# Kernel optimization log

Measured on AMD Instinct MI355X. Metric: run time of the kernel, lower is better.

The kernel has to match this reference:

```python
import jax, jax.numpy as jnp
import numpy as np

N_ENT = 100000
N_REL = 237
DIM = 128
N_EDGE = 500000
BATCH = 4096


def setup_inputs() -> dict:
    key = jax.random.key(0)
    ks = jax.random.split(key, 13)
    s = 0.05
    return {
        "edge_index": jax.random.randint(ks[0], (2, N_EDGE), 0, N_ENT, dtype=jnp.int32),
        "edge_type": jax.random.randint(ks[1], (N_EDGE,), 0, 2 * N_REL, dtype=jnp.int32),
        "sub": jax.random.randint(ks[2], (BATCH,), 0, N_ENT, dtype=jnp.int32),
        "rel": jax.random.randint(ks[3], (BATCH,), 0, 2 * N_REL, dtype=jnp.int32),
        "init_embed_real": jax.random.normal(ks[4], (N_ENT, DIM), jnp.float32) * s,
        "init_embed_imag": jax.random.normal(ks[5], (N_ENT, DIM), jnp.float32) * s,
        "init_rel_real": jax.random.normal(ks[6], (2 * N_REL, DIM), jnp.float32) * s,
        "init_rel_imag": jax.random.normal(ks[7], (2 * N_REL, DIM), jnp.float32) * s,
        "im_proj": jax.random.normal(ks[8], (DIM, DIM), jnp.float32) * s,
        "w_real": jax.random.normal(ks[9], (DIM, DIM), jnp.float32) * s,
        "w_imag": jax.random.normal(ks[10], (DIM, DIM), jnp.float32) * s,
        "w_rel": jax.random.normal(ks[11], (DIM, DIM), jnp.float32) * s,
        "att_a": jax.random.normal(ks[12], (2 * DIM,), jnp.float32) * s,
    }


def _compram_conv(edge_index, edge_type, ent_r, ent_i, rel_r, rel_i,
                  w_real, w_imag, w_rel, att_a):
    """Relational graph-attention conv: complex (ComplEx-style) composition of
    source-entity and relation embeddings per edge, linear projection,
    edge attention with per-destination softmax (segment ops = SpecialSpmm),
    scatter-sum aggregation, tanh activation."""
    src, dst = edge_index[0], edge_index[1]
    er, ei = ent_r[src], ent_i[src]            # [E, D] gathers (irregular)
    rr, ri = rel_r[edge_type], rel_i[edge_type]
    # complex multiplication composition
    m_r = er * rr - ei * ri
    m_i = er * ri + ei * rr
    h_r = m_r @ w_real                          # [E, D]
    h_i = m_i @ w_imag
    logit = jax.nn.leaky_relu(jnp.concatenate([h_r, h_i], axis=-1) @ att_a, 0.2)
    seg_max = jax.ops.segment_max(logit, dst, num_segments=ent_r.shape[0])
    ex = jnp.exp(logit - seg_max[dst])
    denom = jax.ops.segment_sum(ex, dst, num_segments=ent_r.shape[0])
    att = ex / (denom[dst] + 1e-10)             # softmax over incoming edges
    out_r = jax.ops.segment_sum(att[:, None] * h_r, dst, num_segments=ent_r.shape[0])
    out_i = jax.ops.segment_sum(att[:, None] * h_i, dst, num_segments=ent_r.shape[0])
    out_r = jnp.tanh(out_r)
    out_i = jnp.tanh(out_i)
    rel_out_r = jnp.tanh(rel_r @ w_rel)
    rel_out_i = jnp.tanh(rel_i @ w_rel)
    return out_r, out_i, rel_out_r, rel_out_i


def reference(edge_index, edge_type, sub, rel,
              init_embed_real, init_embed_imag,
              init_rel_real, init_rel_imag,
              im_proj, w_real, w_imag, w_rel, att_a):
    # imaginary parts projected through im_proj (as in forward_base)
    rel_i = init_rel_imag @ im_proj
    ent_i = init_embed_imag @ im_proj
    # single CompRAM layer (gcn_layer == 1); dropout is identity in eval mode
    e_r, e_i, r_r, r_i = _compram_conv(edge_index, edge_type,
                                       init_embed_real, ent_i,
                                       init_rel_real, rel_i,
                                       w_real, w_imag, w_rel, att_a)
    sub_r = e_r[sub]
    sub_i = e_i[sub]
    rel_r = r_r[rel]
    rel_i_q = r_i[rel]
    return sub_r, sub_i, rel_r, rel_i_q, e_r, e_i
```

## Files before the change

### kernel.cpp

```cpp
#include <hip/hip_runtime.h>
#include <hip/hip_bf16.h>

#define N_ENT   100000
#define N_RELT  474
#define DIM     128
#define N_EDGE  500000
#define BATCH_Q 4096

typedef __attribute__((ext_vector_type(8))) short short8v;
typedef __attribute__((ext_vector_type(4))) float f32x4;

#define OUT_SUBR 0
#define OUT_SUBI (BATCH_Q * DIM)
#define OUT_RELR (2 * BATCH_Q * DIM)
#define OUT_RELI (3 * BATCH_Q * DIM)
#define OUT_ER   (4 * BATCH_Q * DIM)
#define OUT_EI   (OUT_ER + N_ENT * DIM)

#define WS_ENTI  0
#define WS_RELI  (N_ENT * DIM)
#define WS_RELOR (WS_RELI + N_RELT * DIM)
#define WS_RELOI (WS_RELOR + N_RELT * DIM)
#define WS_DENOM (WS_RELOI + N_RELT * DIM)
#define WS_LIST  (WS_DENOM + N_ENT)
#define WS_CNT2  (WS_LIST + 16384)
#define WS_BSUM  (WS_CNT2 + 64)
#define WS_BF16  (WS_BSUM + 128)

__device__ __forceinline__ unsigned int pack2bf(float a, float b) {
    return (__float_as_uint(a) >> 16) | (__float_as_uint(b) & 0xFFFF0000u);
}
__device__ __forceinline__ unsigned short f2bf(float a) {
    return (unsigned short)(__float_as_uint(a) >> 16);
}
__device__ __forceinline__ float bf2f(unsigned short u) {
    return __uint_as_float(((unsigned int)u) << 16);
}

__global__ void convert_w(const float* __restrict__ P,
                          const float* __restrict__ Wr,
                          const float* __restrict__ Wi,
                          __hip_bfloat16* __restrict__ dst) {
    int i = blockIdx.x * 256 + threadIdx.x;
    if (i < 16384) {
        dst[i] = __float2bfloat16(P[i]);
    } else if (i < 32768) {
        int j = i - 16384; int n = j >> 7, k = j & 127;
        dst[i] = __float2bfloat16(Wr[k * 128 + n]);
    } else if (i < 49152) {
        int j = i - 32768; int n = j >> 7, k = j & 127;
        dst[i] = __float2bfloat16(Wi[k * 128 + n]);
    }
}

__global__ void hist_kernel(const int* __restrict__ eidx, int* __restrict__ cnt) {
    int e = blockIdx.x * 256 + threadIdx.x;
    if (e < N_EDGE) atomicAdd(&cnt[eidx[N_EDGE + e]], 1);
}

__global__ void scan1_kernel(int* __restrict__ cnt, int* __restrict__ bsums) {
    __shared__ int s[1024];
    const int t = threadIdx.x;
    const int gid = blockIdx.x * 1024 + t;
    int v = (gid < N_ENT) ? cnt[gid] : 0;
    s[t] = v;
    __syncthreads();
    for (int off = 1; off < 1024; off <<= 1) {
        int u = (t >= off) ? s[t - off] : 0;
        __syncthreads();
        s[t] += u;
        __syncthreads();
    }
    if (gid < N_ENT) cnt[gid] = s[t] - v;
    if (t == 1023) bsums[blockIdx.x] = s[t];
}

__global__ void scan2_kernel(int* __restrict__ bsums) {
    __shared__ int s[128];
    const int t = threadIdx.x;
    int v = (t < 98) ? bsums[t] : 0;
    s[t] = v;
    __syncthreads();
    for (int off = 1; off < 128; off <<= 1) {
        int u = (t >= off) ? s[t - off] : 0;
        __syncthreads();
        s[t] += u;
        __syncthreads();
    }
    if (t < 98) bsums[t] = s[t] - v;
}

__global__ void scan3_kernel(int* __restrict__ cnt, const int* __restrict__ bsums) {
    const int gid = blockIdx.x * 1024 + threadIdx.x;
    if (gid < N_ENT) cnt[gid] += bsums[blockIdx.x];
}

__global__ void scatter_kernel(const int* __restrict__ eidx,
                               const int* __restrict__ etype,
                               int* __restrict__ cursor,
                               int* __restrict__ sp,
                               int* __restrict__ sd) {
    int e = blockIdx.x * 256 + threadIdx.x;
    if (e >= N_EDGE) return;
    int d = eidx[N_EDGE + e];
    int p = atomicAdd(&cursor[d], 1);
    sp[p] = eidx[e] | (etype[e] << 17);
    sd[p] = d;
}

__launch_bounds__(512, 4)
__global__ void proj_ent(const float* __restrict__ imag,
                         const __hip_bfloat16* __restrict__ Pb,
                         float* __restrict__ ent_i) {
    __shared__ __align__(16) float sx[64 * 128];
    const int t = threadIdx.x;
    const int base = blockIdx.x * 64;
    for (int i = t; i < 64 * 128; i += 512) {
        int r = i >> 7, k = i & 127;
        int gr = base + r;
        sx[i] = (gr < N_ENT) ? imag[(size_t)gr * DIM + k] : 0.f;
    }
    __syncthreads();
    const int lane = t & 63, g = t >> 6;
    const int j0 = lane, j1 = lane + 64;
    float y0[8], y1[8];
#pragma unroll
    for (int e = 0; e < 8; ++e) { y0[e] = 0.f; y1[e] = 0.f; }
    for (int k = 0; k < 128; k += 4) {
        float p0[4], p1[4];
#pragma unroll
        for (int q = 0; q < 4; ++q) {
            p0[q] = __bfloat162float(Pb[(k + q) * 128 + j0]);
            p1[q] = __bfloat162float(Pb[(k + q) * 128 + j1]);
        }
#pragma unroll
        for (int e = 0; e < 8; ++e) {
            const float4 xv = *reinterpret_cast<const float4*>(&sx[(g * 8 + e) * 128 + k]);
            y0[e] = fmaf(xv.x, p0[0], y0[e]); y0[e] = fmaf(xv.y, p0[1], y0[e]);
            y0[e] = fmaf(xv.z, p0[2], y0[e]); y0[e] = fmaf(xv.w, p0[3], y0[e]);
            y1[e] = fmaf(xv.x, p1[0], y1[e]); y1[e] = fmaf(xv.y, p1[1], y1[e]);
            y1[e] = fmaf(xv.z, p1[2], y1[e]); y1[e] = fmaf(xv.w, p1[3], y1[e]);
        }
    }
#pragma unroll
    for (int e = 0; e < 8; ++e) {
        int gr = base + g * 8 + e;
        if (gr < N_ENT) {
            ent_i[(size_t)gr * DIM + j0] = y0[e];
            ent_i[(size_t)gr * DIM + j1] = y1[e];
        }
    }
}

__global__ void rel_kernel(const float* __restrict__ rel_real,
                           const float* __restrict__ rel_imag,
                           const float* __restrict__ P,
                           const float* __restrict__ Wrel,
                           float* __restrict__ rel_i,
                           float* __restrict__ rel_or,
                           float* __restrict__ rel_oi) {
    __shared__ float s_im[128], s_re[128], s_ri[128];
    const int j = threadIdx.x;
    const int r = blockIdx.x;
    s_im[j] = rel_imag[r * 128 + j];
    s_re[j] = rel_real[r * 128 + j];
    __syncthreads();
    float acc = 0.f;
    for (int k = 0; k < 128; ++k) acc = fmaf(s_im[k], P[k * 128 + j], acc);
    rel_i[r * 128 + j] = acc;
    s_ri[j] = acc;
    __syncthreads();
    float ai = 0.f, ar = 0.f;
    for (int k = 0; k < 128; ++k) {
        float w = Wrel[k * 128 + j];
        ai = fmaf(s_ri[k], w, ai);
        ar = fmaf(s_re[k], w, ar);
    }
    rel_oi[r * 128 + j] = tanhf(ai);
    rel_or[r * 128 + j] = tanhf(ar);
}

__launch_bounds__(512, 6)
__global__ void edge_kernel(const int* __restrict__ sp,
                            const int* __restrict__ sd,
                            const float* __restrict__ ent_r,
                            const float* __restrict__ ent_i,
                            const float* __restrict__ rel_r,
                            const float* __restrict__ rel_i,
                            const unsigned short* __restrict__ Wtr,
                            const unsigned short* __restrict__ Wti,
                            const float* __restrict__ att_a,
                            float* __restrict__ num_r,
                            float* __restrict__ num_i,
                            float* __restrict__ denw) {
    __shared__ __align__(16) unsigned short u_sh[16640];
    __shared__ float plog[64][2];
    __shared__ float exl[64];
    __shared__ int s_se[64], s_dst[64];
    __shared__ int s_flags[2];
    unsigned short* m_r_sh = u_sh;
    unsigned short* m_i_sh = u_sh + 8192;

    const int t = threadIdx.x;
    const int base = blockIdx.x * 64;

    if (t < 64) {
        int ge = base + t;
        bool ok = ge < N_EDGE;
        s_se[t]  = ok ? sp[ge] : 0;
        s_dst[t] = ok ? sd[ge] : -1;
    }
    if (t == 0) s_flags[0] = (base > 0 && sd[base - 1] == sd[base]) ? 1 : 0;
    if (t == 1) { int ge = base + 64; s_flags[1] = (ge < N_EDGE && sd[ge - 1] == sd[ge]) ? 1 : 0; }
    __syncthreads();

    for (int it = 0; it < 2; ++it) {
        int i = t + it * 512;
        int e = i >> 4, c = i & 15;
        bool ok = (base + e) < N_EDGE;
        int pk = s_se[e];
        int src = pk & 0x1FFFF, et = pk >> 17;
        const float* pr = ent_r + (size_t)src * DIM + c * 8;
        const float* pi = ent_i + (size_t)src * DIM + c * 8;
        const float* qr = rel_r + (size_t)et * DIM + c * 8;
        const float* qi = rel_i + (size_t)et * DIM + c * 8;
        float4 er0 = reinterpret_cast<const float4*>(pr)[0];
        float4 er1 = reinterpret_cast<const float4*>(pr)[1];
        float4 ei0 = reinterpret_cast<const float4*>(pi)[0];
        float4 ei1 = reinterpret_cast<const float4*>(pi)[1];
        float4 rr0 = reinterpret_cast<const float4*>(qr)[0];
        float4 rr1 = reinterpret_cast<const float4*>(qr)[1];
        float4 ri0 = reinterpret_cast<const float4*>(qi)[0];
        float4 ri1 = reinterpret_cast<const float4*>(qi)[1];
        float r[8], im[8];
        r[0] = er0.x*rr0.x - ei0.x*ri0.x;  im[0] = er0.x*ri0.x + ei0.x*rr0.x;
        r[1] = er0.y*rr0.y - ei0.y*ri0.y;  im[1] = er0.y*ri0.y + ei0.y*rr0.y;
        r[2] = er0.z*rr0.z - ei0.z*ri0.z;  im[2] = er0.z*ri0.z + ei0.z*rr0.z;
        r[3] = er0.w*rr0.w - ei0.w*ri0.w;  im[3] = er0.w*ri0.w + ei0.w*rr0.w;
        r[4] = er1.x*rr1.x - ei1.x*ri1.x;  im[4] = er1.x*ri1.x + ei1.x*rr1.x;
        r[5] = er1.y*rr1.y - ei1.y*ri1.y;  im[5] = er1.y*ri1.y + ei1.y*rr1.y;
        r[6] = er1.z*rr1.z - ei1.z*ri1.z;  im[6] = er1.z*ri1.z + ei1.z*rr1.z;
        r[7] = er1.w*rr1.w - ei1.w*ri1.w;  im[7] = er1.w*ri1.w + ei1.w*rr1.w;
        uint4 ur, ui;
        if (ok) {
            ur.x = pack2bf(r[0], r[1]); ur.y = pack2bf(r[2], r[3]);
            ur.z = pack2bf(r[4], r[5]); ur.w = pack2bf(r[6], r[7]);
            ui.x = pack2bf(im[0], im[1]); ui.y = pack2bf(im[2], im[3]);
            ui.z = pack2bf(im[4], im[5]); ui.w = pack2bf(im[6], im[7]);
        } else {
            ur.x = ur.y = ur.z = ur.w = 0u;
            ui.x = ui.y = ui.z = ui.w = 0u;
        }
        int idx = e * 128 + ((c ^ (e & 15)) << 3);
        *reinterpret_cast<uint4*>(&m_r_sh[idx]) = ur;
        *reinterpret_cast<uint4*>(&m_i_sh[idx]) = ui;
    }
    __syncthreads();

    const int lane = t & 63, g = t >> 6;
    const int mtile = g & 3, ntile = g >> 2;
    const int l15 = lane & 15, l4 = lane >> 4;
    const int arow = mtile * 16 + l15;

    f32x4 accr[4], acci[4];
#pragma unroll
    for (int nf = 0; nf < 4; ++nf) {
        accr[nf] = (f32x4){0.f, 0.f, 0.f, 0.f};
        acci[nf] = (f32x4){0.f, 0.f, 0.f, 0.f};
    }
#pragma unroll
    for (int ks = 0; ks < 4; ++ks) {
        int chunkx = (ks * 4 + l4) ^ l15;
        int aidx = arow * 128 + chunkx * 8;
        short8v a_r = *reinterpret_cast<const short8v*>(&m_r_sh[aidx]);
        short8v a_i = *reinterpret_cast<const short8v*>(&m_i_sh[aidx]);
        int kb = ks * 32 + l4 * 8;
#pragma unroll
        for (int nf = 0; nf < 4; ++nf) {
            int n = ntile * 64 + nf * 16 + l15;
            short8v b_r = *reinterpret_cast<const short8v*>(&Wtr[n * 128 + kb]);
            short8v b_i = *reinterpret_cast<const short8v*>(&Wti[n * 128 + kb]);
            accr[nf] = __builtin_amdgcn_mfma_f32_16x16x32_bf16(a_r, b_r, accr[nf], 0, 0, 0);
            acci[nf] = __builtin_amdgcn_mfma_f32_16x16x32_bf16(a_i, b_i, acci[nf], 0, 0, 0);
        }
    }

    float pj[4] = {0.f, 0.f, 0.f, 0.f};
#pragma unroll
    for (int nf = 0; nf < 4; ++nf) {
        int n = ntile * 64 + nf * 16 + l15;
        float ar = att_a[n], ai = att_a[128 + n];
#pragma unroll
        for (int j = 0; j < 4; ++j)
            pj[j] += accr[nf][j] * ar + acci[nf][j] * ai;
    }
#pragma unroll
    for (int off = 1; off < 16; off <<= 1) {
#pragma unroll
        for (int j = 0; j < 4; ++j) pj[j] += __shfl_xor(pj[j], off, 64);
    }
    if (l15 == 0) {
#pragma unroll
        for (int j = 0; j < 4; ++j)
            plog[mtile * 16 + l4 * 4 + j][ntile] = pj[j];
    }
    __syncthreads();

    if (t < 64) {
        float lg = plog[t][0] + plog[t][1];
        lg = lg > 0.f ? lg : 0.2f * lg;
        exl[t] = expf(lg);
    }
    __syncthreads();

#pragma unroll
    for (int j = 0; j < 4; ++j) {
        int row = mtile * 16 + l4 * 4 + j;
        float w = exl[row];
#pragma unroll
        for (int nf = 0; nf < 4; ++nf) {
            int col = ntile * 64 + nf * 16 + l15;
            u_sh[row * 260 + col]       = f2bf(w * accr[nf][j]);
            u_sh[row * 260 + 128 + col] = f2bf(w * acci[nf][j]);
        }
    }
    __syncthreads();

    if (t < 256) {
        const int c = t;
        const int cc = c & 127;
        float* plane = (c < 128) ? num_r : num_i;
        const int fs = s_flags[0], ls = s_flags[1];
        float num = 0.f, den = 0.f;
        int dprev = -1, rstart = 0;
        for (int r = 0; r < 64; ++r) {
            int d = s_dst[r];
            if (d != dprev) {
                if (dprev >= 0) {
                    if (rstart == 0 && fs) {
                        atomicAdd(&plane[(size_t)dprev * DIM + cc], num);
                        if (c == 0) atomicAdd(&denw[dprev], den);
                    } else {
                        plane[(size_t)dprev * DIM + cc] = tanhf(num / (den + 1e-10f));
                    }
                }
                dprev = d; num = 0.f; den = 0.f; rstart = r;
            }
            num += bf2f(u_sh[r * 260 + c]);
            den += exl[r];
        }
        if (dprev >= 0) {
            bool isb = (rstart == 0 && fs) || ls;
            if (isb) {
                atomicAdd(&plane[(size_t)dprev * DIM + cc], num);
                if (c == 0) atomicAdd(&denw[dprev], den);
            } else {
                plane[(size_t)dprev * DIM + cc] = tanhf(num / (den + 1e-10f));
            }
        }
    }
}

__global__ void classify_kernel(const int* __restrict__ eo,
                                int* __restrict__ list,
                                int* __restrict__ cnt2) {
    int v = blockIdx.x * 256 + threadIdx.x;
    if (v >= N_ENT) return;
    int start = v ? eo[v - 1] : 0;
    int end = eo[v];
    if (end > start && ((start >> 6) != ((end - 1) >> 6))) {
        int i = atomicAdd(cnt2, 1);
        if (i < 16384) list[i] = v;
    }
}

__global__ void boundary_finalize(const int* __restrict__ list,
                                  const int* __restrict__ cnt2,
                                  const float* __restrict__ denw,
                                  float* __restrict__ er,
                                  float* __restrict__ ei) {
    int j = blockIdx.x;
    if (j >= cnt2[0]) return;
    int v = list[j];
    int c = threadIdx.x;
    float den = denw[v] + 1e-10f;
    float* plane = (c < 128) ? er : ei;
    size_t idx = (size_t)v * DIM + (c & 127);
    plane[idx] = tanhf(plane[idx] / den);
}

__global__ void gather_kernel(const int* __restrict__ sub,
                              const int* __restrict__ rel,
                              const float* __restrict__ relor,
                              const float* __restrict__ reloi,
                              float* __restrict__ out) {
    int idx = blockIdx.x * 256 + threadIdx.x;
    if (idx >= 4 * BATCH_Q * 32) return;
    int arr = idx >> 17;
    int rem = idx & 131071;
    int b = rem >> 5, c = rem & 31;
    const float* srcp;
    float* dstp;
    if (arr == 0)      { srcp = out + OUT_ER + (size_t)sub[b] * DIM; dstp = out + OUT_SUBR; }
    else if (arr == 1) { srcp = out + OUT_EI + (size_t)sub[b] * DIM; dstp = out + OUT_SUBI; }
    else if (arr == 2) { srcp = relor + (size_t)rel[b] * DIM;        dstp = out + OUT_RELR; }
    else               { srcp = reloi + (size_t)rel[b] * DIM;        dstp = out + OUT_RELI; }
    reinterpret_cast<float4*>(dstp + (size_t)b * DIM)[c] =
        reinterpret_cast<const float4*>(srcp)[c];
}

extern "C" void kernel_launch(void* const* d_in, const int* in_sizes, int n_in,
                              void* d_out, int out_size, void* d_ws, size_t ws_size,
                              hipStream_t stream) {
    const int*   eidx    = (const int*)d_in[0];
    const int*   etype   = (const int*)d_in[1];
    const int*   sub     = (const int*)d_in[2];
    const int*   rel     = (const int*)d_in[3];
    const float* emb_r   = (const float*)d_in[4];
    const float* emb_i   = (const float*)d_in[5];
    const float* relreal = (const float*)d_in[6];
    const float* relimag = (const float*)d_in[7];
    const float* im_proj = (const float*)d_in[8];
    const float* w_real  = (const float*)d_in[9];
    const float* w_imag  = (const float*)d_in[10];
    const float* w_rel   = (const float*)d_in[11];
    const float* att_a   = (const float*)d_in[12];

    float* out = (float*)d_out;
    float* ws  = (float*)d_ws;
    int*   wsi = (int*)d_ws;

    float* ent_i  = ws + WS_ENTI;
    float* rel_i  = ws + WS_RELI;
    float* relor  = ws + WS_RELOR;
    float* reloi  = ws + WS_RELOI;
    float* denw   = ws + WS_DENOM;
    int*   list   = wsi + WS_LIST;
    int*   cnt2   = wsi + WS_CNT2;
    int*   bsums  = wsi + WS_BSUM;
    __hip_bfloat16* wb  = reinterpret_cast<__hip_bfloat16*>(ws + WS_BF16);
    __hip_bfloat16* Pb  = wb;
    unsigned short* Wtr = reinterpret_cast<unsigned short*>(wb + 16384);
    unsigned short* Wti = reinterpret_cast<unsigned short*>(wb + 32768);

    int* outi = (int*)d_out;
    int* sp = outi;
    int* sd = outi + N_EDGE;
    int* eo = outi + 2 * N_EDGE;

    hipMemsetAsync(out + OUT_ER, 0, (size_t)(2 * N_ENT * DIM) * sizeof(float), stream);
    hipMemsetAsync(denw, 0, (size_t)N_ENT * sizeof(float), stream);
    hipMemsetAsync(eo,   0, (size_t)N_ENT * sizeof(int), stream);
    hipMemsetAsync(cnt2, 0, 64 * sizeof(int), stream);

    convert_w<<<192, 256, 0, stream>>>(im_proj, w_real, w_imag, wb);
    hist_kernel<<<(N_EDGE + 255) / 256, 256, 0, stream>>>(eidx, eo);
    scan1_kernel<<<98, 1024, 0, stream>>>(eo, bsums);
    scan2_kernel<<<1, 128, 0, stream>>>(bsums);
    scan3_kernel<<<98, 1024, 0, stream>>>(eo, bsums);
    scatter_kernel<<<(N_EDGE + 255) / 256, 256, 0, stream>>>(eidx, etype, eo, sp, sd);
    proj_ent<<<1563, 512, 0, stream>>>(emb_i, Pb, ent_i);
    rel_kernel<<<474, 128, 0, stream>>>(relreal, relimag, im_proj, w_rel,
                                        rel_i, relor, reloi);
    edge_kernel<<<7813, 512, 0, stream>>>(sp, sd, emb_r, ent_i,
                                          relreal, rel_i, Wtr, Wti, att_a,
                                          out + OUT_ER, out + OUT_EI, denw);
    classify_kernel<<<(N_ENT + 255) / 256, 256, 0, stream>>>(eo, list, cnt2);
    boundary_finalize<<<7812, 256, 0, stream>>>(list, cnt2, denw,
                                                out + OUT_ER, out + OUT_EI);
    gather_kernel<<<2048, 256, 0, stream>>>(sub, rel, relor, reloi, out);
}
```

Measured before the change: 662.0 us.

## Store gathered embeddings in bf16, retile MFMA, replace full output memset with targeted zeroing

Entity and relation embeddings (real and projected imaginary) are now stored as bf16 in the workspace, so the per-edge gathers move half the bytes. The edge-kernel MFMA mapping changes so each wave owns 16 output columns across all 64 rows, loading each weight fragment once and reusing it across four M tiles. The 100MB memset of the output planes is replaced by classifying nodes before the edge pass and zeroing only empty or block-boundary rows. The cost is an extra conversion pass over ent_real, lower input precision, and more scratch data kept in the output buffer.

```diff
diff --git a/kernel.cpp b/kernel.cpp
--- a/kernel.cpp
+++ b/kernel.cpp
@@ -16,16 +16,22 @@
 #define OUT_RELI (3 * BATCH_Q * DIM)
 #define OUT_ER   (4 * BATCH_Q * DIM)
 #define OUT_EI   (OUT_ER + N_ENT * DIM)
-
-#define WS_ENTI  0
-#define WS_RELI  (N_ENT * DIM)
-#define WS_RELOR (WS_RELI + N_RELT * DIM)
+#define SC_SP    0
+#define SC_SD    N_EDGE
+#define SC_EO    (2 * N_EDGE)
+#define SC_BLIST (2 * N_EDGE + N_ENT)
+#define SC_ZLIST (SC_BLIST + 16384)
+#define SC_CNT   (SC_ZLIST + 16384)
+#define SC_BSUM  (SC_CNT + 64)
+
+#define WS_ENTIB 0
+#define WS_ENTRB (N_ENT * DIM / 2)
+#define WS_RELRB (2 * (N_ENT * DIM / 2))
+#define WS_RELIB (WS_RELRB + N_RELT * DIM / 2)
+#define WS_RELOR (WS_RELIB + N_RELT * DIM / 2)
 #define WS_RELOI (WS_RELOR + N_RELT * DIM)
 #define WS_DENOM (WS_RELOI + N_RELT * DIM)
-#define WS_LIST  (WS_DENOM + N_ENT)
-#define WS_CNT2  (WS_LIST + 16384)
-#define WS_BSUM  (WS_CNT2 + 64)
-#define WS_BF16  (WS_BSUM + 128)
+#define WS_BF16  (WS_DENOM + N_ENT)
 
 __device__ __forceinline__ unsigned int pack2bf(float a, float b) {
     return (__float_as_uint(a) >> 16) | (__float_as_uint(b) & 0xFFFF0000u);
@@ -40,17 +46,29 @@
 __global__ void convert_w(const float* __restrict__ P,
                           const float* __restrict__ Wr,
                           const float* __restrict__ Wi,
-                          __hip_bfloat16* __restrict__ dst) {
+                          unsigned short* __restrict__ dst) {
     int i = blockIdx.x * 256 + threadIdx.x;
     if (i < 16384) {
-        dst[i] = __float2bfloat16(P[i]);
+        dst[i] = f2bf(P[i]);
     } else if (i < 32768) {
         int j = i - 16384; int n = j >> 7, k = j & 127;
-        dst[i] = __float2bfloat16(Wr[k * 128 + n]);
+        dst[i] = f2bf(Wr[k * 128 + n]);
     } else if (i < 49152) {
         int j = i - 32768; int n = j >> 7, k = j & 127;
-        dst[i] = __float2bfloat16(Wi[k * 128 + n]);
-    }
+        dst[i] = f2bf(Wi[k * 128 + n]);
+    }
+}
+
+__global__ void convert_entr(const float* __restrict__ src,
+                             unsigned short* __restrict__ dst) {
+    int i = blockIdx.x * 256 + threadIdx.x;
+    if (i >= N_ENT * DIM / 8) return;
+    const float4* s4 = reinterpret_cast<const float4*>(src);
+    float4 a = s4[2 * i], b = s4[2 * i + 1];
+    uint4 o;
+    o.x = pack2bf(a.x, a.y); o.y = pack2bf(a.z, a.w);
+    o.z = pack2bf(b.x, b.y); o.w = pack2bf(b.z, b.w);
+    reinterpret_cast<uint4*>(dst)[i] = o;
 }
 
 __global__ void hist_kernel(const int* __restrict__ eidx, int* __restrict__ cnt) {
@@ -93,6 +111,31 @@
 __global__ void scan3_kernel(int* __restrict__ cnt, const int* __restrict__ bsums) {
     const int gid = blockIdx.x * 1024 + threadIdx.x;
     if (gid < N_ENT) cnt[gid] += bsums[blockIdx.x];
+}
+
+__global__ void classify_pre(const int* __restrict__ eo,
+                             int* __restrict__ blist,
+                             int* __restrict__ zlist,
+                             int* __restrict__ cnts) {
+    int v = blockIdx.x * 256 + threadIdx.x;
+    if (v >= N_ENT) return;
+    int start = eo[v];
+    int end = (v == N_ENT - 1) ? N_EDGE : eo[v + 1];
+    bool empty = (end == start);
+    bool bound = (end > start) && ((start >> 6) != ((end - 1) >> 6));
+    if (bound) { int i = atomicAdd(&cnts[0], 1); if (i < 16384) blist[i] = v; }
+    if (empty || bound) { int i = atomicAdd(&cnts[1], 1); if (i < 16384) zlist[i] = v; }
+}
+
+__global__ void zero_rows(const int* __restrict__ zlist,
+                          const int* __restrict__ cnts,
+                          float* __restrict__ er, float* __restrict__ ei) {
+    int j = blockIdx.x;
+    if (j >= cnts[1]) return;
+    int v = zlist[j];
+    int c = threadIdx.x;
+    float* plane = (c < 128) ? er : ei;
+    plane[(size_t)v * DIM + (c & 127)] = 0.f;
 }
 
 __global__ void scatter_kernel(const int* __restrict__ eidx,
@@ -110,8 +153,8 @@
 
 __launch_bounds__(512, 4)
 __global__ void proj_ent(const float* __restrict__ imag,
-                         const __hip_bfloat16* __restrict__ Pb,
-                         float* __restrict__ ent_i) {
+                         const unsigned short* __restrict__ Pb,
+                         unsigned short* __restrict__ ent_ib) {
     __shared__ __align__(16) float sx[64 * 128];
     const int t = threadIdx.x;
     const int base = blockIdx.x * 64;
@@ -122,7 +165,6 @@
     }
     __syncthreads();
     const int lane = t & 63, g = t >> 6;
-    const int j0 = lane, j1 = lane + 64;
     float y0[8], y1[8];
 #pragma unroll
     for (int e = 0; e < 8; ++e) { y0[e] = 0.f; y1[e] = 0.f; }
@@ -130,8 +172,9 @@
         float p0[4], p1[4];
 #pragma unroll
         for (int q = 0; q < 4; ++q) {
-            p0[q] = __bfloat162float(Pb[(k + q) * 128 + j0]);
-            p1[q] = __bfloat162float(Pb[(k + q) * 128 + j1]);
+            unsigned int up = *reinterpret_cast<const unsigned int*>(&Pb[(k + q) * 128 + 2 * lane]);
+            p0[q] = bf2f((unsigned short)(up & 0xFFFFu));
+            p1[q] = bf2f((unsigned short)(up >> 16));
         }
 #pragma unroll
         for (int e = 0; e < 8; ++e) {
@@ -145,10 +188,9 @@
 #pragma unroll
     for (int e = 0; e < 8; ++e) {
         int gr = base + g * 8 + e;
-        if (gr < N_ENT) {
-            ent_i[(size_t)gr * DIM + j0] = y0[e];
-            ent_i[(size_t)gr * DIM + j1] = y1[e];
-        }
+        if (gr < N_ENT)
+            *reinterpret_cast<unsigned int*>(&ent_ib[(size_t)gr * DIM + 2 * lane]) =
+                pack2bf(y0[e], y1[e]);
     }
 }
 
@@ -156,7 +198,8 @@
                            const float* __restrict__ rel_imag,
                            const float* __restrict__ P,
                            const float* __restrict__ Wrel,
-                           float* __restrict__ rel_i,
+                           unsigned short* __restrict__ rel_rb,
+                           unsigned short* __restrict__ rel_ib,
                            float* __restrict__ rel_or,
                            float* __restrict__ rel_oi) {
     __shared__ float s_im[128], s_re[128], s_ri[128];
@@ -167,7 +210,8 @@
     __syncthreads();
     float acc = 0.f;
     for (int k = 0; k < 128; ++k) acc = fmaf(s_im[k], P[k * 128 + j], acc);
-    rel_i[r * 128 + j] = acc;
+    rel_ib[r * 128 + j] = f2bf(acc);
+    rel_rb[r * 128 + j] = f2bf(s_re[j]);
     s_ri[j] = acc;
     __syncthreads();
     float ai = 0.f, ar = 0.f;
@@ -180,13 +224,21 @@
     rel_or[r * 128 + j] = tanhf(ar);
 }
 
+#define COMPOSE(eru, eiu, rru, riu, mro, mio) {                                   \
+    float er_a = __uint_as_float((eru) << 16), er_b = __uint_as_float((eru) & 0xFFFF0000u); \
+    float ei_a = __uint_as_float((eiu) << 16), ei_b = __uint_as_float((eiu) & 0xFFFF0000u); \
+    float rr_a = __uint_as_float((rru) << 16), rr_b = __uint_as_float((rru) & 0xFFFF0000u); \
+    float ri_a = __uint_as_float((riu) << 16), ri_b = __uint_as_float((riu) & 0xFFFF0000u); \
+    mro = pack2bf(er_a * rr_a - ei_a * ri_a, er_b * rr_b - ei_b * ri_b);          \
+    mio = pack2bf(er_a * ri_a + ei_a * rr_a, er_b * ri_b + ei_b * rr_b); }
+
 __launch_bounds__(512, 6)
 __global__ void edge_kernel(const int* __restrict__ sp,
                             const int* __restrict__ sd,
-                            const float* __restrict__ ent_r,
-                            const float* __restrict__ ent_i,
-                            const float* __restrict__ rel_r,
-                            const float* __restrict__ rel_i,
+                            const unsigned short* __restrict__ ent_rb,
+                            const unsigned short* __restrict__ ent_ib,
+                            const unsigned short* __restrict__ rel_rb,
+                            const unsigned short* __restrict__ rel_ib,
                             const unsigned short* __restrict__ Wtr,
                             const unsigned short* __restrict__ Wti,
                             const float* __restrict__ att_a,
@@ -194,7 +246,7 @@
                             float* __restrict__ num_i,
                             float* __restrict__ denw) {
     __shared__ __align__(16) unsigned short u_sh[16640];
-    __shared__ float plog[64][2];
+    __shared__ float plog[64][8];
     __shared__ float exl[64];
     __shared__ int s_se[64], s_dst[64];
     __shared__ int s_flags[2];
@@ -220,110 +272,89 @@
         bool ok = (base + e) < N_EDGE;
         int pk = s_se[e];
         int src = pk & 0x1FFFF, et = pk >> 17;
-        const float* pr = ent_r + (size_t)src * DIM + c * 8;
-        const float* pi = ent_i + (size_t)src * DIM + c * 8;
-        const float* qr = rel_r + (size_t)et * DIM + c * 8;
-        const float* qi = rel_i + (size_t)et * DIM + c * 8;
-        float4 er0 = reinterpret_cast<const float4*>(pr)[0];
-        float4 er1 = reinterpret_cast<const float4*>(pr)[1];
-        float4 ei0 = reinterpret_cast<const float4*>(pi)[0];
-        float4 ei1 = reinterpret_cast<const float4*>(pi)[1];
-        float4 rr0 = reinterpret_cast<const float4*>(qr)[0];
-        float4 rr1 = reinterpret_cast<const float4*>(qr)[1];
-        float4 ri0 = reinterpret_cast<const float4*>(qi)[0];
-        float4 ri1 = reinterpret_cast<const float4*>(qi)[1];
-        float r[8], im[8];
-        r[0] = er0.x*rr0.x - ei0.x*ri0.x;  im[0] = er0.x*ri0.x + ei0.x*rr0.x;
-        r[1] = er0.y*rr0.y - ei0.y*ri0.y;  im[1] = er0.y*ri0.y + ei0.y*rr0.y;
-        r[2] = er0.z*rr0.z - ei0.z*ri0.z;  im[2] = er0.z*ri0.z + ei0.z*rr0.z;
-        r[3] = er0.w*rr0.w - ei0.w*ri0.w;  im[3] = er0.w*ri0.w + ei0.w*rr0.w;
-        r[4] = er1.x*rr1.x - ei1.x*ri1.x;  im[4] = er1.x*ri1.x + ei1.x*rr1.x;
-        r[5] = er1.y*rr1.y - ei1.y*ri1.y;  im[5] = er1.y*ri1.y + ei1.y*rr1.y;
-        r[6] = er1.z*rr1.z - ei1.z*ri1.z;  im[6] = er1.z*ri1.z + ei1.z*rr1.z;
-        r[7] = er1.w*rr1.w - ei1.w*ri1.w;  im[7] = er1.w*ri1.w + ei1.w*rr1.w;
-        uint4 ur, ui;
-        if (ok) {
-            ur.x = pack2bf(r[0], r[1]); ur.y = pack2bf(r[2], r[3]);
-            ur.z = pack2bf(r[4], r[5]); ur.w = pack2bf(r[6], r[7]);
-            ui.x = pack2bf(im[0], im[1]); ui.y = pack2bf(im[2], im[3]);
-            ui.z = pack2bf(im[4], im[5]); ui.w = pack2bf(im[6], im[7]);
-        } else {
-            ur.x = ur.y = ur.z = ur.w = 0u;
-            ui.x = ui.y = ui.z = ui.w = 0u;
-        }
+        uint4 erv = *reinterpret_cast<const uint4*>(&ent_rb[(size_t)src * DIM + c * 8]);
+        uint4 eiv = *reinterpret_cast<const uint4*>(&ent_ib[(size_t)src * DIM + c * 8]);
+        uint4 rrv = *reinterpret_cast<const uint4*>(&rel_rb[et * DIM + c * 8]);
+        uint4 riv = *reinterpret_cast<const uint4*>(&rel_ib[et * DIM + c * 8]);
+        uint4 mr, mi;
+        COMPOSE(erv.x, eiv.x, rrv.x, riv.x, mr.x, mi.x);
+        COMPOSE(erv.y, eiv.y, rrv.y, riv.y, mr.y, mi.y);
+        COMPOSE(erv.z, eiv.z, rrv.z, riv.z, mr.z, mi.z);
+        COMPOSE(erv.w, eiv.w, rrv.w, riv.w, mr.w, mi.w);
+        if (!ok) { mr.x = mr.y = mr.z = mr.w = 0u; mi.x = mi.y = mi.z = mi.w = 0u; }
         int idx = e * 128 + ((c ^ (e & 15)) << 3);
-        *reinterpret_cast<uint4*>(&m_r_sh[idx]) = ur;
-        *reinterpret_cast<uint4*>(&m_i_sh[idx]) = ui;
+        *reinterpret_cast<uint4*>(&m_r_sh[idx]) = mr;
+        *reinterpret_cast<uint4*>(&m_i_sh[idx]) = mi;
     }
     __syncthreads();
 
     const int lane = t & 63, g = t >> 6;
-    const int mtile = g & 3, ntile = g >> 2;
     const int l15 = lane & 15, l4 = lane >> 4;
-    const int arow = mtile * 16 + l15;
+    const int ncol = g * 16 + l15;
 
     f32x4 accr[4], acci[4];
 #pragma unroll
-    for (int nf = 0; nf < 4; ++nf) {
-        accr[nf] = (f32x4){0.f, 0.f, 0.f, 0.f};
-        acci[nf] = (f32x4){0.f, 0.f, 0.f, 0.f};
+    for (int mt = 0; mt < 4; ++mt) {
+        accr[mt] = (f32x4){0.f, 0.f, 0.f, 0.f};
+        acci[mt] = (f32x4){0.f, 0.f, 0.f, 0.f};
     }
 #pragma unroll
     for (int ks = 0; ks < 4; ++ks) {
+        int kb = ks * 32 + l4 * 8;
+        short8v b_r = *reinterpret_cast<const short8v*>(&Wtr[ncol * 128 + kb]);
+        short8v b_i = *reinterpret_cast<const short8v*>(&Wti[ncol * 128 + kb]);
         int chunkx = (ks * 4 + l4) ^ l15;
-        int aidx = arow * 128 + chunkx * 8;
-        short8v a_r = *reinterpret_cast<const short8v*>(&m_r_sh[aidx]);
-        short8v a_i = *reinterpret_cast<const short8v*>(&m_i_sh[aidx]);
-        int kb = ks * 32 + l4 * 8;
-#pragma unroll
-        for (int nf = 0; nf < 4; ++nf) {
-            int n = ntile * 64 + nf * 16 + l15;
-            short8v b_r = *reinterpret_cast<const short8v*>(&Wtr[n * 128 + kb]);
-            short8v b_i = *reinterpret_cast<const short8v*>(&Wti[n * 128 + kb]);
-            accr[nf] = __builtin_amdgcn_mfma_f32_16x16x32_bf16(a_r, b_r, accr[nf], 0, 0, 0);
-            acci[nf] = __builtin_amdgcn_mfma_f32_16x16x32_bf16(a_i, b_i, acci[nf], 0, 0, 0);
-        }
-    }
-
-    float pj[4] = {0.f, 0.f, 0.f, 0.f};
-#pragma unroll
-    for (int nf = 0; nf < 4; ++nf) {
-        int n = ntile * 64 + nf * 16 + l15;
-        float ar = att_a[n], ai = att_a[128 + n];
+#pragma unroll
+        for (int mt = 0; mt < 4; ++mt) {
+            int aidx = (mt * 16 + l15) * 128 + chunkx * 8;
+            short8v a_r = *reinterpret_cast<const short8v*>(&m_r_sh[aidx]);
+            short8v a_i = *reinterpret_cast<const short8v*>(&m_i_sh[aidx]);
+            accr[mt] = __builtin_amdgcn_mfma_f32_16x16x32_bf16(a_r, b_r, accr[mt], 0, 0, 0);
+            acci[mt] = __builtin_amdgcn_mfma_f32_16x16x32_bf16(a_i, b_i, acci[mt], 0, 0, 0);
+        }
+    }
+
+    const float a_r = att_a[ncol], a_i = att_a[128 + ncol];
+    float pj[4][4];
+#pragma unroll
+    for (int mt = 0; mt < 4; ++mt)
 #pragma unroll
         for (int j = 0; j < 4; ++j)
-            pj[j] += accr[nf][j] * ar + acci[nf][j] * ai;
-    }
+            pj[mt][j] = accr[mt][j] * a_r + acci[mt][j] * a_i;
 #pragma unroll
     for (int off = 1; off < 16; off <<= 1) {
 #pragma unroll
-        for (int j = 0; j < 4; ++j) pj[j] += __shfl_xor(pj[j], off, 64);
+        for (int mt = 0; mt < 4; ++mt)
+#pragma unroll
+            for (int j = 0; j < 4; ++j)
+                pj[mt][j] += __shfl_xor(pj[mt][j], off, 64);
     }
     if (l15 == 0) {
 #pragma unroll
-        for (int j = 0; j < 4; ++j)
-            plog[mtile * 16 + l4 * 4 + j][ntile] = pj[j];
+        for (int mt = 0; mt < 4; ++mt)
+#pragma unroll
+            for (int j = 0; j < 4; ++j)
+                plog[mt * 16 + l4 * 4 + j][g] = pj[mt][j];
     }
     __syncthreads();
 
     if (t < 64) {
-        float lg = plog[t][0] + plog[t][1];
+        float lg = plog[t][0] + plog[t][1] + plog[t][2] + plog[t][3]
+                 + plog[t][4] + plog[t][5] + plog[t][6] + plog[t][7];
         lg = lg > 0.f ? lg : 0.2f * lg;
         exl[t] = expf(lg);
     }
     __syncthreads();
 
 #pragma unroll
-    for (int j = 0; j < 4; ++j) {
-        int row = mtile * 16 + l4 * 4 + j;
-        float w = exl[row];
-#pragma unroll
-        for (int nf = 0; nf < 4; ++nf) {
-            int col = ntile * 64 + nf * 16 + l15;
-            u_sh[row * 260 + col]       = f2bf(w * accr[nf][j]);
-            u_sh[row * 260 + 128 + col] = f2bf(w * acci[nf][j]);
-        }
-    }
+    for (int mt = 0; mt < 4; ++mt)
+#pragma unroll
+        for (int j = 0; j < 4; ++j) {
+            int row = mt * 16 + l4 * 4 + j;
+            float w = exl[row];
+            u_sh[row * 260 + ncol]       = f2bf(w * accr[mt][j]);
+            u_sh[row * 260 + 128 + ncol] = f2bf(w * acci[mt][j]);
+        }
     __syncthreads();
 
     if (t < 256) {
@@ -361,27 +392,14 @@
     }
 }
 
-__global__ void classify_kernel(const int* __restrict__ eo,
-                                int* __restrict__ list,
-                                int* __restrict__ cnt2) {
-    int v = blockIdx.x * 256 + threadIdx.x;
-    if (v >= N_ENT) return;
-    int start = v ? eo[v - 1] : 0;
-    int end = eo[v];
-    if (end > start && ((start >> 6) != ((end - 1) >> 6))) {
-        int i = atomicAdd(cnt2, 1);
-        if (i < 16384) list[i] = v;
-    }
-}
-
-__global__ void boundary_finalize(const int* __restrict__ list,
-                                  const int* __restrict__ cnt2,
+__global__ void boundary_finalize(const int* __restrict__ blist,
+                                  const int* __restrict__ cnts,
                                   const float* __restrict__ denw,
                                   float* __restrict__ er,
                                   float* __restrict__ ei) {
     int j = blockIdx.x;
-    if (j >= cnt2[0]) return;
-    int v = list[j];
+    if (j >= cnts[0]) return;
+    int v = blist[j];
     int c = threadIdx.x;
     float den = denw[v] + 1e-10f;
     float* plane = (c < 128) ? er : ei;
@@ -428,45 +446,48 @@
 
     float* out = (float*)d_out;
     float* ws  = (float*)d_ws;
-    int*   wsi = (int*)d_ws;
-
-    float* ent_i  = ws + WS_ENTI;
-    float* rel_i  = ws + WS_RELI;
+
+    unsigned short* ent_ib = reinterpret_cast<unsigned short*>(ws + WS_ENTIB);
+    unsigned short* ent_rb = reinterpret_cast<unsigned short*>(ws + WS_ENTRB);
+    unsigned short* rel_rb = reinterpret_cast<unsigned short*>(ws + WS_RELRB);
+    unsigned short* rel_ib = reinterpret_cast<unsigned short*>(ws + WS_RELIB);
     float* relor  = ws + WS_RELOR;
     float* reloi  = ws + WS_RELOI;
     float* denw   = ws + WS_DENOM;
-    int*   list   = wsi + WS_LIST;
-    int*   cnt2   = wsi + WS_CNT2;
-    int*   bsums  = wsi + WS_BSUM;
-    __hip_bfloat16* wb  = reinterpret_cast<__hip_bfloat16*>(ws + WS_BF16);
-    __hip_bfloat16* Pb  = wb;
-    unsigned short* Wtr = reinterpret_cast<unsigned short*>(wb + 16384);
-    unsigned short* Wti = reinterpret_cast<unsigned short*>(wb + 32768);
-
-    int* outi = (int*)d_out;
-    int* sp = outi;
-    int* sd = outi + N_EDGE;
-    int* eo = outi + 2 * N_EDGE;
-
-    hipMemsetAsync(out + OUT_ER, 0, (size_t)(2 * N_ENT * DIM) * sizeof(float), stream);
+    unsigned short* wb  = reinterpret_cast<unsigned short*>(ws + WS_BF16);
+    unsigned short* Pb  = wb;
+    unsigned short* Wtr = wb + 16384;
+    unsigned short* Wti = wb + 32768;
+
+    int* outi  = (int*)d_out;
+    int* sp    = outi + SC_SP;
+    int* sd    = outi + SC_SD;
+    int* eo    = outi + SC_EO;
+    int* blist = outi + SC_BLIST;
+    int* zlist = outi + SC_ZLIST;
+    int* cnts  = outi + SC_CNT;
+    int* bsums = outi + SC_BSUM;
+
     hipMemsetAsync(denw, 0, (size_t)N_ENT * sizeof(float), stream);
     hipMemsetAsync(eo,   0, (size_t)N_ENT * sizeof(int), stream);
-    hipMemsetAsync(cnt2, 0, 64 * sizeof(int), stream);
+    hipMemsetAsync(cnts, 0, 64 * sizeof(int), stream);
 
     convert_w<<<192, 256, 0, stream>>>(im_proj, w_real, w_imag, wb);
+    convert_entr<<<6250, 256, 0, stream>>>(emb_r, ent_rb);
     hist_kernel<<<(N_EDGE + 255) / 256, 256, 0, stream>>>(eidx, eo);
     scan1_kernel<<<98, 1024, 0, stream>>>(eo, bsums);
     scan2_kernel<<<1, 128, 0, stream>>>(bsums);
     scan3_kernel<<<98, 1024, 0, stream>>>(eo, bsums);
+    classify_pre<<<(N_ENT + 255) / 256, 256, 0, stream>>>(eo, blist, zlist, cnts);
+    zero_rows<<<16384, 256, 0, stream>>>(zlist, cnts, out + OUT_ER, out + OUT_EI);
     scatter_kernel<<<(N_EDGE + 255) / 256, 256, 0, stream>>>(eidx, etype, eo, sp, sd);
-    proj_ent<<<1563, 512, 0, stream>>>(emb_i, Pb, ent_i);
+    proj_ent<<<1563, 512, 0, stream>>>(emb_i, Pb, ent_ib);
     rel_kernel<<<474, 128, 0, stream>>>(relreal, relimag, im_proj, w_rel,
-                                        rel_i, relor, reloi);
-    edge_kernel<<<7813, 512, 0, stream>>>(sp, sd, emb_r, ent_i,
-                                          relreal, rel_i, Wtr, Wti, att_a,
+                                        rel_rb, rel_ib, relor, reloi);
+    edge_kernel<<<7813, 512, 0, stream>>>(sp, sd, ent_rb, ent_ib,
+                                          rel_rb, rel_ib, Wtr, Wti, att_a,
                                           out + OUT_ER, out + OUT_EI, denw);
-    classify_kernel<<<(N_ENT + 255) / 256, 256, 0, stream>>>(eo, list, cnt2);
-    boundary_finalize<<<7812, 256, 0, stream>>>(list, cnt2, denw,
+    boundary_finalize<<<8192, 256, 0, stream>>>(blist, cnts, denw,
                                                 out + OUT_ER, out + OUT_EI);
     gather_kernel<<<2048, 256, 0, stream>>>(sub, rel, relor, reloi, out);
 }
```

New measurement: 570.8 us. -13.8%, faster.
